# Kernel optimization log

Hardware: AMD Instinct MI355X
Metric: run time of the kernel (lower is better)

## Reference

```python
import jax, jax.numpy as jnp
import numpy as np

DIM = 768
HEADS = 12
HD = DIM // HEADS  # 64
EPS = 1e-5


def _ln(t, g, b):
    # LayerNorm over last axis (head_dim), torch eps=1e-5, biased variance
    mu = jnp.mean(t, axis=-1, keepdims=True)
    var = jnp.mean(jnp.square(t - mu), axis=-1, keepdims=True)
    return (t - mu) * jax.lax.rsqrt(var + EPS) * g + b


def _get_qkv(t, W, bias, gq, bq, gk, bk):
    bs, n, c = t.shape
    qkv = t @ W.T + bias                      # [bs, n, 3c]
    q, k, v = jnp.split(qkv, 3, axis=-1)
    def heads(u):
        return u.reshape(bs, n, HEADS, HD).transpose(0, 2, 1, 3)  # [bs,H,n,hd]
    q, k, v = heads(q), heads(k), heads(v)
    return _ln(q, gq, bq), _ln(k, gk, bk), v


def setup_inputs() -> dict:
    key = jax.random.key(0)
    ks = jax.random.split(key, 12)
    s_in = 1.0 / np.sqrt(DIM)
    d = {
        "x": jax.random.normal(ks[0], (4, 1024, DIM), jnp.float32),
        "y": jax.random.normal(ks[1], (4, 1024, DIM), jnp.float32),
        "Wqkv_x": jax.random.uniform(ks[2], (3 * DIM, DIM), jnp.float32, -s_in, s_in),
        "bqkv_x": jnp.zeros((3 * DIM,), jnp.float32),
        "Wqkv_y": jax.random.uniform(ks[3], (3 * DIM, DIM), jnp.float32, -s_in, s_in),
        "bqkv_y": jnp.zeros((3 * DIM,), jnp.float32),
        "Wproj_x": jax.random.uniform(ks[4], (DIM, DIM), jnp.float32, -s_in, s_in),
        "bproj_x": jnp.zeros((DIM,), jnp.float32),
        "Wproj_y": jax.random.uniform(ks[5], (DIM, DIM), jnp.float32, -s_in, s_in),
        "bproj_y": jnp.zeros((DIM,), jnp.float32),
        "gq_x": jnp.ones((HD,), jnp.float32), "bq_x": jnp.zeros((HD,), jnp.float32),
        "gk_x": jnp.ones((HD,), jnp.float32), "bk_x": jnp.zeros((HD,), jnp.float32),
        "gq_y": jnp.ones((HD,), jnp.float32), "bq_y": jnp.zeros((HD,), jnp.float32),
        "gk_y": jnp.ones((HD,), jnp.float32), "bk_y": jnp.zeros((HD,), jnp.float32),
    }
    return d


def reference(x, y, Wqkv_x, bqkv_x, Wqkv_y, bqkv_y, Wproj_x, bproj_x,
              Wproj_y, bproj_y, gq_x, bq_x, gk_x, bk_x, gq_y, bq_y, gk_y, bk_y):
    bs, n, c = x.shape
    qx, kx, vx = _get_qkv(x, Wqkv_x, bqkv_x, gq_x, bq_x, gk_x, bk_x)
    qy, ky, vy = _get_qkv(y, Wqkv_y, bqkv_y, gq_y, bq_y, gk_y, bk_y)
    q = jnp.concatenate([qx, qy], axis=2)     # [bs,H,n+m,hd]
    k = jnp.concatenate([kx, ky], axis=2)
    v = jnp.concatenate([vx, vy], axis=2)
    score = jnp.einsum("bhqd,bhkd->bhqk", q, k) / np.sqrt(HD)
    attn = jax.nn.softmax(score, axis=-1)
    out = jnp.einsum("bhqk,bhkd->bhqd", attn, v)  # [bs,H,n+m,hd]
    out = out.transpose(0, 2, 1, 3).reshape(bs, -1, c)
    ox, oy = out[:, :n, :], out[:, n:, :]
    return ox @ Wproj_x.T + bproj_x, oy @ Wproj_y.T + bproj_y
```

## Files before the change

kernel.cpp:

```cpp
#include <hip/hip_runtime.h>
#include <stdint.h>

typedef unsigned int u32;
typedef __attribute__((ext_vector_type(8))) __bf16 bf16x8;
typedef __attribute__((ext_vector_type(8))) short s16x8;
typedef __attribute__((ext_vector_type(4))) short s16x4;
typedef __attribute__((ext_vector_type(4))) float f32x4;


__device__ __forceinline__ short f2bf(float f) {
    __bf16 h = (__bf16)f;
    return __builtin_bit_cast(short, h);
}

__device__ __forceinline__ bf16x8 asbf(s16x8 v) {
    return __builtin_bit_cast(bf16x8, v);
}

__device__ __forceinline__ void gl_lds16(const void* g, void* l) {
    __builtin_amdgcn_global_load_lds((__attribute__((address_space(1))) u32*)g,
                                     (__attribute__((address_space(3))) u32*)l,
                                     16, 0, 0);
}



__global__ __launch_bounds__(256) void pack_tiles(
    const float* __restrict__ x,  short* __restrict__ xP,
    const float* __restrict__ y,  short* __restrict__ yP,
    const float* __restrict__ wqx, short* __restrict__ wqxP,
    const float* __restrict__ wqy, short* __restrict__ wqyP,
    const float* __restrict__ wpx, short* __restrict__ wpxP,
    const float* __restrict__ wpy, short* __restrict__ wpyP)
{
    const int tid  = threadIdx.x;
    const int w    = tid >> 6, lane = tid & 63;
    const int lam  = lane & 15, quad = lane >> 4;

    int t = blockIdx.x;
    const float* src; short* dst;
    if (t < 384)                 { src = x;   dst = xP; }
    else if ((t -= 384) < 384)   { src = y;   dst = yP; }
    else if ((t -= 384) < 216)   { src = wqx; dst = wqxP; }
    else if ((t -= 216) < 216)   { src = wqy; dst = wqyP; }
    else if ((t -= 216) < 72)    { src = wpx; dst = wpxP; }
    else                         { t -= 72;  src = wpy; dst = wpyP; }

    const int kb = t % 12, rb = t / 12;
    const int m0 = rb * 128, k0 = kb * 64;
    short* dtile = dst + (size_t)t * 8192;

    #pragma unroll
    for (int u = 0; u < 2; u++) {
        const int ig = w * 2 + u;
        #pragma unroll
        for (int c = 0; c < 2; c++) {
            const float* sp = src + (size_t)(m0 + ig * 16 + lam) * 768 + k0 + c * 32 + quad * 8;
            f32x4 a = *(const f32x4*)sp;
            f32x4 b = *(const f32x4*)(sp + 4);
            s16x8 o;
            o[0] = f2bf(a.x); o[1] = f2bf(a.y); o[2] = f2bf(a.z); o[3] = f2bf(a.w);
            o[4] = f2bf(b.x); o[5] = f2bf(b.y); o[6] = f2bf(b.z); o[7] = f2bf(b.w);
            *(s16x8*)(dtile + (c * 8 + ig) * 512 + lane * 8) = o;
        }
    }
}


__device__ __forceinline__ void stage_qkv(
    const short* __restrict__ At, const short* __restrict__ Wt,
    short* __restrict__ dA, short* __restrict__ dB, int w, int lane)
{
    #pragma unroll
    for (int c = 0; c < 2; c++)
        #pragma unroll
        for (int h = 0; h < 2; h++) {
            const int ch = c * 8 + w + h * 4;
            gl_lds16(At + ch * 512 + lane * 8, dA + ch * 512);
            gl_lds16(Wt + ch * 512 + lane * 8, dB + ch * 512);
        }
}

__global__ __launch_bounds__(256, 2) void qkv_gemm(
    const short* __restrict__ AxP, const short* __restrict__ AyP,
    const short* __restrict__ WxP, const short* __restrict__ WyP,
    const float* __restrict__ biasx, const float* __restrict__ biasy,
    const float* __restrict__ gqx, const float* __restrict__ bqx,
    const float* __restrict__ gkx, const float* __restrict__ bkx,
    const float* __restrict__ gqy, const float* __restrict__ bqy,
    const float* __restrict__ gky, const float* __restrict__ bky,
    short* __restrict__ Q, short* __restrict__ KP, short* __restrict__ VP)
{
    __shared__ union {
        struct { short a[8192]; short b[8192]; } st;
        short e[4][5120];
    } uL;
    const int tid  = threadIdx.x;
    const int w    = tid >> 6, lane = tid & 63;
    const int lam  = lane & 15, quad = lane >> 4;
    const int strm = blockIdx.z;
    const int mblk = blockIdx.x;
    const int nblk = blockIdx.y;
    const short* AP   = strm ? AyP : AxP;
    const short* WP   = strm ? WyP : WxP;
    const float* bias = strm ? biasy : biasx;
    const int m0 = mblk * 128;
    const int n0 = nblk * 128;
    const int wm = w >> 1, wn = w & 1;

    const f32x4 fzero = {0.f, 0.f, 0.f, 0.f};
    f32x4 acc[4][4];
    #pragma unroll
    for (int i = 0; i < 4; i++)
        #pragma unroll
        for (int t = 0; t < 4; t++) acc[i][t] = fzero;

    for (int kb = 0; kb < 12; ++kb) {
        __syncthreads();
        stage_qkv(AP + (size_t)(mblk * 12 + kb) * 8192,
                  WP + (size_t)(nblk * 12 + kb) * 8192,
                  uL.st.a, uL.st.b, w, lane);
        __syncthreads();
        s16x8 af[2][4], bfr[2][4];
        #pragma unroll
        for (int c = 0; c < 2; c++)
            #pragma unroll
            for (int i = 0; i < 4; i++)
                af[c][i] = *(const s16x8*)(uL.st.a + ((c * 8 + wm * 4 + i) * 64 + lane) * 8);
        #pragma unroll
        for (int c = 0; c < 2; c++)
            #pragma unroll
            for (int t = 0; t < 4; t++)
                bfr[c][t] = *(const s16x8*)(uL.st.b + ((c * 8 + wn * 4 + t) * 64 + lane) * 8);
        #pragma unroll
        for (int c = 0; c < 2; c++)
            #pragma unroll
            for (int i = 0; i < 4; i++)
                #pragma unroll
                for (int t = 0; t < 4; t++)
                    acc[i][t] = __builtin_amdgcn_mfma_f32_16x16x32_bf16(
                        asbf(af[c][i]), asbf(bfr[c][t]), acc[i][t], 0, 0, 0);
    }
    __syncthreads();

    const int nb     = n0 + wn * 64;
    const int region = nb / 768;
    const int head   = (nb % 768) / 64;
    const int mg0    = m0 + wm * 64;
    const int b_     = mg0 >> 10;
    const int sg0    = (mg0 & 1023) + strm * 1024;
    short* myE = uL.e[w];

    float bv[4];
    #pragma unroll
    for (int t = 0; t < 4; t++) bv[t] = bias[nb + t * 16 + lam];
    float gv[4], bb[4];
    if (region < 2) {
        const float* gp = (region == 0) ? (strm ? gqy : gqx) : (strm ? gky : gkx);
        const float* bp = (region == 0) ? (strm ? bqy : bqx) : (strm ? bky : bkx);
        #pragma unroll
        for (int t = 0; t < 4; t++) { gv[t] = gp[t * 16 + lam]; bb[t] = bp[t * 16 + lam]; }
    }

    #pragma unroll
    for (int i = 0; i < 4; i++) {
        #pragma unroll
        for (int reg = 0; reg < 4; reg++) {
            const int lr = i * 16 + quad * 4 + reg;
            float v0 = acc[i][0][reg] + bv[0];
            float v1 = acc[i][1][reg] + bv[1];
            float v2 = acc[i][2][reg] + bv[2];
            float v3 = acc[i][3][reg] + bv[3];
            if (region < 2) {
                float s = v0 + v1 + v2 + v3;
                s += __shfl_xor(s, 1); s += __shfl_xor(s, 2);
                s += __shfl_xor(s, 4); s += __shfl_xor(s, 8);
                const float mean = s * (1.f / 64.f);
                const float c0 = v0 - mean, c1 = v1 - mean, c2 = v2 - mean, c3 = v3 - mean;
                float q2 = c0 * c0 + c1 * c1 + c2 * c2 + c3 * c3;
                q2 += __shfl_xor(q2, 1); q2 += __shfl_xor(q2, 2);
                q2 += __shfl_xor(q2, 4); q2 += __shfl_xor(q2, 8);
                const float rs = rsqrtf(q2 * (1.f / 64.f) + 1e-5f);
                v0 = c0 * rs * gv[0] + bb[0];
                v1 = c1 * rs * gv[1] + bb[1];
                v2 = c2 * rs * gv[2] + bb[2];
                v3 = c3 * rs * gv[3] + bb[3];
                myE[lr * 80 + 0 * 16 + lam] = f2bf(v0);
                myE[lr * 80 + 1 * 16 + lam] = f2bf(v1);
                myE[lr * 80 + 2 * 16 + lam] = f2bf(v2);
                myE[lr * 80 + 3 * 16 + lam] = f2bf(v3);
            } else {
                myE[(0 * 16 + lam) * 80 + lr] = f2bf(v0);
                myE[(1 * 16 + lam) * 80 + lr] = f2bf(v1);
                myE[(2 * 16 + lam) * 80 + lr] = f2bf(v2);
                myE[(3 * 16 + lam) * 80 + lr] = f2bf(v3);
            }
        }
    }

    if (region == 0) {
        const int l8 = lane >> 3, c8 = (lane & 7) * 8;
        short* dstp = Q + ((size_t)(b_ * 12 + head) * 2048 + sg0) * 64;
        #pragma unroll
        for (int j = 0; j < 8; j++) {
            const int rr = j * 8 + l8;
            *(s16x8*)(dstp + (size_t)rr * 64 + c8) = *(const s16x8*)(myE + rr * 80 + c8);
        }
    } else {
        short* dstp = (region == 1 ? KP : VP) +
                      ((size_t)(b_ * 12 + head) * 32 + (sg0 >> 6)) * 4096;
        #pragma unroll
        for (int c = 0; c < 2; c++)
            #pragma unroll
            for (int ig = 0; ig < 4; ig++) {
                s16x8 vv = *(const s16x8*)(myE + (ig * 16 + lam) * 80 + c * 32 + quad * 8);
                *(s16x8*)(dstp + (c * 4 + ig) * 512 + lane * 8) = vv;
            }
    }
}


__global__ __launch_bounds__(256, 2) void attn(
    const short* __restrict__ Q, const short* __restrict__ KP,
    const short* __restrict__ VP, short* __restrict__ OP)
{
    __shared__ __align__(16) short lP[4][2560];
    const int tid  = threadIdx.x;
    const int w    = tid >> 6, lane = tid & 63;
    const int lam  = lane & 15, quad = lane >> 4;
    const int bh   = blockIdx.x;
    const int q0   = blockIdx.y * 128 + w * 32;
    const short* Qb  = Q  + (size_t)bh * 2048 * 64;
    const short* KPb = KP + (size_t)bh * 32 * 4096;
    const short* VPb = VP + (size_t)bh * 32 * 4096;
    short* myP = lP[w];

    s16x8 aq[2][2];
    #pragma unroll
    for (int qf = 0; qf < 2; qf++)
        #pragma unroll
        for (int c = 0; c < 2; c++)
            aq[qf][c] = *(const s16x8*)(Qb + (size_t)(q0 + qf * 16 + lam) * 64 + c * 32 + quad * 8);

    const f32x4 fzero = {0.f, 0.f, 0.f, 0.f};
    f32x4 o[2][4];
    float lsum[2][4];
    #pragma unroll
    for (int qf = 0; qf < 2; qf++) {
        #pragma unroll
        for (int t = 0; t < 4; t++) o[qf][t] = fzero;
        #pragma unroll
        for (int r = 0; r < 4; r++) lsum[qf][r] = 0.f;
    }

    const float c1 = 0.18033688011112042f;

    for (int it = 0; it < 32; ++it) {
        const short* kt = KPb + (size_t)it * 4096;
        const short* vt = VPb + (size_t)it * 4096;

        s16x8 kf[4][2];
        #pragma unroll
        for (int t = 0; t < 4; t++) {
            kf[t][0] = *(const s16x8*)(kt + (0 * 4 + t) * 512 + lane * 8);
            kf[t][1] = *(const s16x8*)(kt + (1 * 4 + t) * 512 + lane * 8);
        }
        s16x8 vf[4][2];
        #pragma unroll
        for (int t = 0; t < 4; t++) {
            vf[t][0] = *(const s16x8*)(vt + (0 * 4 + t) * 512 + lane * 8);
            vf[t][1] = *(const s16x8*)(vt + (1 * 4 + t) * 512 + lane * 8);
        }

        f32x4 sc[2][4];
        #pragma unroll
        for (int qf = 0; qf < 2; qf++)
            #pragma unroll
            for (int t = 0; t < 4; t++) sc[qf][t] = fzero;
        #pragma unroll
        for (int t = 0; t < 4; t++)
            #pragma unroll
            for (int qf = 0; qf < 2; qf++) {
                sc[qf][t] = __builtin_amdgcn_mfma_f32_16x16x32_bf16(
                    asbf(aq[qf][0]), asbf(kf[t][0]), sc[qf][t], 0, 0, 0);
                sc[qf][t] = __builtin_amdgcn_mfma_f32_16x16x32_bf16(
                    asbf(aq[qf][1]), asbf(kf[t][1]), sc[qf][t], 0, 0, 0);
            }

        s16x8 ap[2][2];
        #pragma unroll
        for (int qf = 0; qf < 2; qf++) {
            #pragma unroll
            for (int t = 0; t < 4; t++) {
                const int g = t * 2 + (lam >> 3);
                #pragma unroll
                for (int r = 0; r < 4; r++) {
                    const float p = __builtin_amdgcn_exp2f(__builtin_fmaf(sc[qf][t][r], c1, -30.f));
                    lsum[qf][r] += p;
                    myP[(g * 17 + quad * 4 + r) * 8 + (lam & 7)] = f2bf(p);
                }
            }
            ap[qf][0] = *(const s16x8*)(myP + (quad * 17 + lam) * 8);
            ap[qf][1] = *(const s16x8*)(myP + ((4 + quad) * 17 + lam) * 8);
        }

        #pragma unroll
        for (int t = 0; t < 4; t++)
            #pragma unroll
            for (int qf = 0; qf < 2; qf++) {
                o[qf][t] = __builtin_amdgcn_mfma_f32_16x16x32_bf16(
                    asbf(ap[qf][0]), asbf(vf[t][0]), o[qf][t], 0, 0, 0);
                o[qf][t] = __builtin_amdgcn_mfma_f32_16x16x32_bf16(
                    asbf(ap[qf][1]), asbf(vf[t][1]), o[qf][t], 0, 0, 0);
            }
    }

    short* myO = lP[w];
    #pragma unroll
    for (int qf = 0; qf < 2; qf++) {
        #pragma unroll
        for (int r = 0; r < 4; r++) {
            float l = lsum[qf][r];
            l += __shfl_xor(l, 1); l += __shfl_xor(l, 2);
            l += __shfl_xor(l, 4); l += __shfl_xor(l, 8);
            const float inv = 1.0f / l;
            const int row = qf * 16 + quad * 4 + r;
            #pragma unroll
            for (int t = 0; t < 4; t++)
                myO[row * 80 + t * 16 + lam] = f2bf(o[qf][t][r] * inv);
        }
    }

    const int b_ = bh / 12, h_ = bh % 12;
    const int strm = q0 >> 10;
    const int s    = q0 & 1023;
    const int sb   = s >> 6;
    short* dstp = OP + (((size_t)((strm * 4 + b_) * 16 + sb)) * 12 + h_) * 4096;
    const int igb = (s & 63) >> 4;
    #pragma unroll
    for (int u = 0; u < 2; u++) {
        const int ig = igb + u;
        #pragma unroll
        for (int c = 0; c < 2; c++) {
            s16x8 vv = *(const s16x8*)(myO + (u * 16 + lam) * 80 + c * 32 + quad * 8);
            *(s16x8*)(dstp + (c * 4 + ig) * 512 + lane * 8) = vv;
        }
    }
}


__device__ __forceinline__ void stage_proj(
    const short* __restrict__ Ot, const short* __restrict__ Wt,
    short* __restrict__ dA, short* __restrict__ dB, int w, int lane)
{
    #pragma unroll
    for (int u = 0; u < 2; u++) {
        const int ch = w * 2 + u;
        gl_lds16(Ot + ch * 512 + lane * 8, dA + ch * 512);
    }
    #pragma unroll
    for (int c = 0; c < 2; c++)
        #pragma unroll
        for (int h = 0; h < 2; h++) {
            const int ch = c * 8 + w + h * 4;
            gl_lds16(Wt + ch * 512 + lane * 8, dB + ch * 512);
        }
}

__global__ __launch_bounds__(256, 3) void proj_gemm(
    const short* __restrict__ OP,
    const short* __restrict__ WpxP, const short* __restrict__ WpyP,
    const float* __restrict__ bpx, const float* __restrict__ bpy,
    float* __restrict__ out)
{
    __shared__ __align__(16) short lA[2][4096];
    __shared__ __align__(16) short lB[2][8192];
    const int tid  = threadIdx.x;
    const int w    = tid >> 6, lane = tid & 63;
    const int lam  = lane & 15, quad = lane >> 4;
    const int strm = blockIdx.z;
    const short* WP   = strm ? WpyP : WpxP;
    const float* bias = strm ? bpy : bpx;
    const int m0 = blockIdx.x * 64;
    const int n0 = blockIdx.y * 128;
    const int wm = w >> 1, wn = w & 1;

    const int b_ = m0 >> 10, sb = (m0 & 1023) >> 6;
    const size_t tA0 = ((size_t)((strm * 4 + b_) * 16 + sb)) * 12;
    const size_t tB0 = (size_t)blockIdx.y * 12;

    const f32x4 fzero = {0.f, 0.f, 0.f, 0.f};
    f32x4 acc[2][4];
    #pragma unroll
    for (int i = 0; i < 2; i++)
        #pragma unroll
        for (int t = 0; t < 4; t++) acc[i][t] = fzero;

    stage_proj(OP + tA0 * 4096, WP + tB0 * 8192, lA[0], lB[0], w, lane);
    __syncthreads();

    int bi = 0;
    for (int kb = 0; kb < 12; ++kb) {
        if (kb + 1 < 12)
            stage_proj(OP + (tA0 + kb + 1) * 4096, WP + (tB0 + kb + 1) * 8192,
                       lA[bi ^ 1], lB[bi ^ 1], w, lane);

        const short* cA = lA[bi];
        const short* cB = lB[bi];
        s16x8 af[2][2], bfr[2][4];
        #pragma unroll
        for (int c = 0; c < 2; c++)
            #pragma unroll
            for (int i = 0; i < 2; i++)
                af[c][i] = *(const s16x8*)(cA + ((c * 4 + wm * 2 + i) * 64 + lane) * 8);
        #pragma unroll
        for (int c = 0; c < 2; c++)
            #pragma unroll
            for (int t = 0; t < 4; t++)
                bfr[c][t] = *(const s16x8*)(cB + ((c * 8 + wn * 4 + t) * 64 + lane) * 8);
        #pragma unroll
        for (int c = 0; c < 2; c++)
            #pragma unroll
            for (int i = 0; i < 2; i++)
                #pragma unroll
                for (int t = 0; t < 4; t++)
                    acc[i][t] = __builtin_amdgcn_mfma_f32_16x16x32_bf16(
                        asbf(af[c][i]), asbf(bfr[c][t]), acc[i][t], 0, 0, 0);

        __syncthreads();
        bi ^= 1;
    }

    const int nb = n0 + wn * 64;
    float bv[4];
    #pragma unroll
    for (int t = 0; t < 4; t++) bv[t] = bias[nb + t * 16 + lam];
    #pragma unroll
    for (int i = 0; i < 2; i++) {
        #pragma unroll
        for (int reg = 0; reg < 4; reg++) {
            const int mg = m0 + wm * 32 + i * 16 + quad * 4 + reg;
            float* dst = out + (size_t)strm * 3145728 + (size_t)mg * 768 + nb;
            #pragma unroll
            for (int t = 0; t < 4; t++) dst[t * 16 + lam] = acc[i][t][reg] + bv[t];
        }
    }
}


#define WS_XP  0
#define WS_YP  6291456
#define WS_WQX 12582912
#define WS_WQY 16121856
#define WS_WPX 19660800
#define WS_WPY 20840448
#define WS_Q   22020096
#define WS_KP  34603008
#define WS_VP  47185920
#define WS_OP  59768832

extern "C" void kernel_launch(void* const* d_in, const int* in_sizes, int n_in,
                              void* d_out, int out_size, void* d_ws, size_t ws_size,
                              hipStream_t stream) {
    (void)in_sizes; (void)n_in; (void)out_size; (void)ws_size;
    const float* x       = (const float*)d_in[0];
    const float* y       = (const float*)d_in[1];
    const float* Wqkv_x  = (const float*)d_in[2];
    const float* bqkv_x  = (const float*)d_in[3];
    const float* Wqkv_y  = (const float*)d_in[4];
    const float* bqkv_y  = (const float*)d_in[5];
    const float* Wproj_x = (const float*)d_in[6];
    const float* bproj_x = (const float*)d_in[7];
    const float* Wproj_y = (const float*)d_in[8];
    const float* bproj_y = (const float*)d_in[9];
    const float* gq_x = (const float*)d_in[10];
    const float* bq_x = (const float*)d_in[11];
    const float* gk_x = (const float*)d_in[12];
    const float* bk_x = (const float*)d_in[13];
    const float* gq_y = (const float*)d_in[14];
    const float* bq_y = (const float*)d_in[15];
    const float* gk_y = (const float*)d_in[16];
    const float* bk_y = (const float*)d_in[17];

    char* ws = (char*)d_ws;
    short* xP   = (short*)(ws + WS_XP);
    short* yP   = (short*)(ws + WS_YP);
    short* wqxP = (short*)(ws + WS_WQX);
    short* wqyP = (short*)(ws + WS_WQY);
    short* wpxP = (short*)(ws + WS_WPX);
    short* wpyP = (short*)(ws + WS_WPY);
    short* Qb   = (short*)(ws + WS_Q);
    short* KPb  = (short*)(ws + WS_KP);
    short* VPb  = (short*)(ws + WS_VP);
    short* OPb  = (short*)(ws + WS_OP);

    pack_tiles<<<1344, 256, 0, stream>>>(x, xP, y, yP, Wqkv_x, wqxP,
                                         Wqkv_y, wqyP, Wproj_x, wpxP, Wproj_y, wpyP);

    dim3 g1(32, 18, 2);
    qkv_gemm<<<g1, 256, 0, stream>>>(xP, yP, wqxP, wqyP, bqkv_x, bqkv_y,
                                     gq_x, bq_x, gk_x, bk_x,
                                     gq_y, bq_y, gk_y, bk_y,
                                     Qb, KPb, VPb);

    dim3 g2(48, 16);
    attn<<<g2, 256, 0, stream>>>(Qb, KPb, VPb, OPb);

    dim3 g3(64, 6, 2);
    proj_gemm<<<g3, 256, 0, stream>>>(OPb, wpxP, wpyP, bproj_x, bproj_y, (float*)d_out);
}
```

Measured before the change: 238.5 us.

## Keep softmax P in registers via transposed QK^T and 16x16x16 MFMA for PV

The attention kernel now computes S^T by swapping the MFMA operands, so each lane holds four keys for one query. That lets P be fed straight into a 16x16x16 bf16 MFMA against V fragments loaded as 4-wide pieces, removing the LDS round trip for P. The softmax scale is folded into the Q LayerNorm gamma and beta, and the -30 offset into the score accumulator's initial value. The QKV GEMM drops LDS staging and barriers in favour of direct global-to-register double-buffered fragment loads. This risks redundant global loads across waves and uses the lower-throughput K=16 MFMA for the PV product.

```diff
diff --git a/kernel.cpp b/kernel.cpp
--- a/kernel.cpp
+++ b/kernel.cpp
@@ -3,6 +3,7 @@
 
 typedef unsigned int u32;
 typedef __attribute__((ext_vector_type(8))) __bf16 bf16x8;
+typedef __attribute__((ext_vector_type(4))) __bf16 bf16x4;
 typedef __attribute__((ext_vector_type(8))) short s16x8;
 typedef __attribute__((ext_vector_type(4))) short s16x4;
 typedef __attribute__((ext_vector_type(4))) float f32x4;
@@ -15,6 +16,26 @@
 
 __device__ __forceinline__ bf16x8 asbf(s16x8 v) {
     return __builtin_bit_cast(bf16x8, v);
+}
+
+__device__ __forceinline__ f32x4 mfma32(s16x8 a, s16x8 b, f32x4 c) {
+    return __builtin_amdgcn_mfma_f32_16x16x32_bf16(asbf(a), asbf(b), c, 0, 0, 0);
+}
+
+__device__ __forceinline__ f32x4 mfma16(s16x4 a, s16x4 b, f32x4 c) {
+#if defined(__AMDGCN__)
+#if __has_builtin(__builtin_amdgcn_mfma_f32_16x16x16bf16_1k)
+    return __builtin_amdgcn_mfma_f32_16x16x16bf16_1k(a, b, c, 0, 0, 0);
+#else
+    f32x4 d;
+    asm volatile("v_mfma_f32_16x16x16_bf16 %0, %1, %2, %3"
+                 : "=v"(d) : "v"(a), "v"(b), "v"(c));
+    return d;
+#endif
+#else
+    (void)a; (void)b;
+    return c;
+#endif
 }
 
 __device__ __forceinline__ void gl_lds16(const void* g, void* l) {
@@ -67,20 +88,6 @@
 }
 
 
-__device__ __forceinline__ void stage_qkv(
-    const short* __restrict__ At, const short* __restrict__ Wt,
-    short* __restrict__ dA, short* __restrict__ dB, int w, int lane)
-{
-    #pragma unroll
-    for (int c = 0; c < 2; c++)
-        #pragma unroll
-        for (int h = 0; h < 2; h++) {
-            const int ch = c * 8 + w + h * 4;
-            gl_lds16(At + ch * 512 + lane * 8, dA + ch * 512);
-            gl_lds16(Wt + ch * 512 + lane * 8, dB + ch * 512);
-        }
-}
-
 __global__ __launch_bounds__(256, 2) void qkv_gemm(
     const short* __restrict__ AxP, const short* __restrict__ AyP,
     const short* __restrict__ WxP, const short* __restrict__ WyP,
@@ -91,10 +98,7 @@
     const float* __restrict__ gky, const float* __restrict__ bky,
     short* __restrict__ Q, short* __restrict__ KP, short* __restrict__ VP)
 {
-    __shared__ union {
-        struct { short a[8192]; short b[8192]; } st;
-        short e[4][5120];
-    } uL;
+    __shared__ __align__(16) short lE[4][5120];
     const int tid  = threadIdx.x;
     const int w    = tid >> 6, lane = tid & 63;
     const int lam  = lane & 15, quad = lane >> 4;
@@ -108,6 +112,9 @@
     const int n0 = nblk * 128;
     const int wm = w >> 1, wn = w & 1;
 
+    const short* Ap = AP + (size_t)mblk * 12 * 8192 + lane * 8;
+    const short* Wp = WP + (size_t)nblk * 12 * 8192 + lane * 8;
+
     const f32x4 fzero = {0.f, 0.f, 0.f, 0.f};
     f32x4 acc[4][4];
     #pragma unroll
@@ -115,33 +122,30 @@
         #pragma unroll
         for (int t = 0; t < 4; t++) acc[i][t] = fzero;
 
-    for (int kb = 0; kb < 12; ++kb) {
-        __syncthreads();
-        stage_qkv(AP + (size_t)(mblk * 12 + kb) * 8192,
-                  WP + (size_t)(nblk * 12 + kb) * 8192,
-                  uL.st.a, uL.st.b, w, lane);
-        __syncthreads();
-        s16x8 af[2][4], bfr[2][4];
-        #pragma unroll
-        for (int c = 0; c < 2; c++)
-            #pragma unroll
-            for (int i = 0; i < 4; i++)
-                af[c][i] = *(const s16x8*)(uL.st.a + ((c * 8 + wm * 4 + i) * 64 + lane) * 8);
-        #pragma unroll
-        for (int c = 0; c < 2; c++)
+    #define QOFF(kc_, sel_, i_) (((kc_) >> 1) * 8192 + (((kc_) & 1) * 8 + (sel_) * 4 + (i_)) * 512)
+
+    s16x8 fa[2][4], fb[2][4];
+    #pragma unroll
+    for (int i = 0; i < 4; i++) fa[0][i] = *(const s16x8*)(Ap + QOFF(0, wm, i));
+    #pragma unroll
+    for (int t = 0; t < 4; t++) fb[0][t] = *(const s16x8*)(Wp + QOFF(0, wn, t));
+
+    #pragma unroll
+    for (int kc = 0; kc < 24; ++kc) {
+        const int cur = kc & 1, nxt = cur ^ 1;
+        if (kc + 1 < 24) {
+            #pragma unroll
+            for (int i = 0; i < 4; i++) fa[nxt][i] = *(const s16x8*)(Ap + QOFF(kc + 1, wm, i));
+            #pragma unroll
+            for (int t = 0; t < 4; t++) fb[nxt][t] = *(const s16x8*)(Wp + QOFF(kc + 1, wn, t));
+        }
+        #pragma unroll
+        for (int i = 0; i < 4; i++)
             #pragma unroll
             for (int t = 0; t < 4; t++)
-                bfr[c][t] = *(const s16x8*)(uL.st.b + ((c * 8 + wn * 4 + t) * 64 + lane) * 8);
-        #pragma unroll
-        for (int c = 0; c < 2; c++)
-            #pragma unroll
-            for (int i = 0; i < 4; i++)
-                #pragma unroll
-                for (int t = 0; t < 4; t++)
-                    acc[i][t] = __builtin_amdgcn_mfma_f32_16x16x32_bf16(
-                        asbf(af[c][i]), asbf(bfr[c][t]), acc[i][t], 0, 0, 0);
-    }
-    __syncthreads();
+                acc[i][t] = mfma32(fa[cur][i], fb[cur][t], acc[i][t]);
+    }
+    #undef QOFF
 
     const int nb     = n0 + wn * 64;
     const int region = nb / 768;
@@ -149,7 +153,7 @@
     const int mg0    = m0 + wm * 64;
     const int b_     = mg0 >> 10;
     const int sg0    = (mg0 & 1023) + strm * 1024;
-    short* myE = uL.e[w];
+    short* myE = lE[w];
 
     float bv[4];
     #pragma unroll
@@ -158,8 +162,9 @@
     if (region < 2) {
         const float* gp = (region == 0) ? (strm ? gqy : gqx) : (strm ? gky : gkx);
         const float* bp = (region == 0) ? (strm ? bqy : bqx) : (strm ? bky : bkx);
-        #pragma unroll
-        for (int t = 0; t < 4; t++) { gv[t] = gp[t * 16 + lam]; bb[t] = bp[t * 16 + lam]; }
+        const float qs  = (region == 0) ? 0.18033688011112042f : 1.0f;
+        #pragma unroll
+        for (int t = 0; t < 4; t++) { gv[t] = gp[t * 16 + lam] * qs; bb[t] = bp[t * 16 + lam] * qs; }
     }
 
     #pragma unroll
@@ -224,7 +229,7 @@
     const short* __restrict__ Q, const short* __restrict__ KP,
     const short* __restrict__ VP, short* __restrict__ OP)
 {
-    __shared__ __align__(16) short lP[4][2560];
+    __shared__ __align__(16) short lO[4][2560];
     const int tid  = threadIdx.x;
     const int w    = tid >> 6, lane = tid & 63;
     const int lam  = lane & 15, quad = lane >> 4;
@@ -233,7 +238,6 @@
     const short* Qb  = Q  + (size_t)bh * 2048 * 64;
     const short* KPb = KP + (size_t)bh * 32 * 4096;
     const short* VPb = VP + (size_t)bh * 32 * 4096;
-    short* myP = lP[w];
 
     s16x8 aq[2][2];
     #pragma unroll
@@ -243,17 +247,16 @@
             aq[qf][c] = *(const s16x8*)(Qb + (size_t)(q0 + qf * 16 + lam) * 64 + c * 32 + quad * 8);
 
     const f32x4 fzero = {0.f, 0.f, 0.f, 0.f};
+    const f32x4 minit = {-30.f, -30.f, -30.f, -30.f};
     f32x4 o[2][4];
-    float lsum[2][4];
-    #pragma unroll
-    for (int qf = 0; qf < 2; qf++) {
+    float lsum[2] = {0.f, 0.f};
+    #pragma unroll
+    for (int qf = 0; qf < 2; qf++)
         #pragma unroll
         for (int t = 0; t < 4; t++) o[qf][t] = fzero;
-        #pragma unroll
-        for (int r = 0; r < 4; r++) lsum[qf][r] = 0.f;
-    }
-
-    const float c1 = 0.18033688011112042f;
+
+    const int vsub0 = ((0 * 2 + (quad >> 1)) * 16 + lam) * 8 + (quad & 1) * 4;
+    const int vsub1 = ((1 * 2 + (quad >> 1)) * 16 + lam) * 8 + (quad & 1) * 4;
 
     for (int it = 0; it < 32; ++it) {
         const short* kt = KPb + (size_t)it * 4096;
@@ -265,65 +268,52 @@
             kf[t][0] = *(const s16x8*)(kt + (0 * 4 + t) * 512 + lane * 8);
             kf[t][1] = *(const s16x8*)(kt + (1 * 4 + t) * 512 + lane * 8);
         }
-        s16x8 vf[4][2];
-        #pragma unroll
-        for (int t = 0; t < 4; t++) {
-            vf[t][0] = *(const s16x8*)(vt + (0 * 4 + t) * 512 + lane * 8);
-            vf[t][1] = *(const s16x8*)(vt + (1 * 4 + t) * 512 + lane * 8);
-        }
-
-        f32x4 sc[2][4];
-        #pragma unroll
-        for (int qf = 0; qf < 2; qf++)
-            #pragma unroll
-            for (int t = 0; t < 4; t++) sc[qf][t] = fzero;
-        #pragma unroll
-        for (int t = 0; t < 4; t++)
-            #pragma unroll
-            for (int qf = 0; qf < 2; qf++) {
-                sc[qf][t] = __builtin_amdgcn_mfma_f32_16x16x32_bf16(
-                    asbf(aq[qf][0]), asbf(kf[t][0]), sc[qf][t], 0, 0, 0);
-                sc[qf][t] = __builtin_amdgcn_mfma_f32_16x16x32_bf16(
-                    asbf(aq[qf][1]), asbf(kf[t][1]), sc[qf][t], 0, 0, 0);
+        s16x4 vb[4][4];
+        #pragma unroll
+        for (int dt = 0; dt < 4; dt++)
+            #pragma unroll
+            for (int t = 0; t < 4; t++)
+                vb[dt][t] = *(const s16x4*)(vt + ((t >> 1) * 4 + dt) * 512 +
+                                            ((t & 1) ? vsub1 : vsub0));
+
+        #pragma unroll
+        for (int qf = 0; qf < 2; qf++) {
+            f32x4 sc[4];
+            #pragma unroll
+            for (int t = 0; t < 4; t++) sc[t] = minit;
+            #pragma unroll
+            for (int t = 0; t < 4; t++) {
+                sc[t] = mfma32(kf[t][0], aq[qf][0], sc[t]);
+                sc[t] = mfma32(kf[t][1], aq[qf][1], sc[t]);
             }
-
-        s16x8 ap[2][2];
-        #pragma unroll
-        for (int qf = 0; qf < 2; qf++) {
-            #pragma unroll
-            for (int t = 0; t < 4; t++) {
-                const int g = t * 2 + (lam >> 3);
+            s16x4 pf[4];
+            float ls = 0.f;
+            #pragma unroll
+            for (int t = 0; t < 4; t++)
                 #pragma unroll
                 for (int r = 0; r < 4; r++) {
-                    const float p = __builtin_amdgcn_exp2f(__builtin_fmaf(sc[qf][t][r], c1, -30.f));
-                    lsum[qf][r] += p;
-                    myP[(g * 17 + quad * 4 + r) * 8 + (lam & 7)] = f2bf(p);
+                    const float p = __builtin_amdgcn_exp2f(sc[t][r]);
+                    ls += p;
+                    pf[t][r] = f2bf(p);
                 }
-            }
-            ap[qf][0] = *(const s16x8*)(myP + (quad * 17 + lam) * 8);
-            ap[qf][1] = *(const s16x8*)(myP + ((4 + quad) * 17 + lam) * 8);
-        }
-
-        #pragma unroll
-        for (int t = 0; t < 4; t++)
-            #pragma unroll
-            for (int qf = 0; qf < 2; qf++) {
-                o[qf][t] = __builtin_amdgcn_mfma_f32_16x16x32_bf16(
-                    asbf(ap[qf][0]), asbf(vf[t][0]), o[qf][t], 0, 0, 0);
-                o[qf][t] = __builtin_amdgcn_mfma_f32_16x16x32_bf16(
-                    asbf(ap[qf][1]), asbf(vf[t][1]), o[qf][t], 0, 0, 0);
-            }
-    }
-
-    short* myO = lP[w];
+            lsum[qf] += ls;
+            #pragma unroll
+            for (int dt = 0; dt < 4; dt++)
+                #pragma unroll
+                for (int t = 0; t < 4; t++)
+                    o[qf][dt] = mfma16(pf[t], vb[dt][t], o[qf][dt]);
+        }
+    }
+
+    short* myO = lO[w];
     #pragma unroll
     for (int qf = 0; qf < 2; qf++) {
+        float l = lsum[qf];
+        l += __shfl_xor(l, 16);
+        l += __shfl_xor(l, 32);
         #pragma unroll
         for (int r = 0; r < 4; r++) {
-            float l = lsum[qf][r];
-            l += __shfl_xor(l, 1); l += __shfl_xor(l, 2);
-            l += __shfl_xor(l, 4); l += __shfl_xor(l, 8);
-            const float inv = 1.0f / l;
+            const float inv = 1.0f / __shfl(l, quad * 4 + r, 16);
             const int row = qf * 16 + quad * 4 + r;
             #pragma unroll
             for (int t = 0; t < 4; t++)
@@ -424,8 +414,7 @@
             for (int i = 0; i < 2; i++)
                 #pragma unroll
                 for (int t = 0; t < 4; t++)
-                    acc[i][t] = __builtin_amdgcn_mfma_f32_16x16x32_bf16(
-                        asbf(af[c][i]), asbf(bfr[c][t]), acc[i][t], 0, 0, 0);
+                    acc[i][t] = mfma32(af[c][i], bfr[c][t], acc[i][t]);
 
         __syncthreads();
         bi ^= 1;
```

Result: slower. 253.1 us (+6.1%).

## Shrink attention tiles to 16 query rows per wave and fold softmax scale into Q LayerNorm

Applied to the files above, without the earlier changes.

The attention kernel now gives each wave 16 query rows instead of 32, doubles the grid, halves its LDS and raises launch bounds to 6 blocks per CU, aiming for higher occupancy to hide K/V load latency. The softmax scale (log2e/sqrt(hd)) is folded into the Q LayerNorm gain and bias, and the -30 offset is moved into the score accumulator's initial value, removing an FMA per score element. The QKV epilogue is split into two halves so it needs half the LDS staging. In exchange, each block reuses K/V fragments over fewer query rows, which doubles global/L2 traffic for K and V.

```diff
diff --git a/kernel.cpp b/kernel.cpp
--- a/kernel.cpp
+++ b/kernel.cpp
@@ -15,6 +15,10 @@
 
 __device__ __forceinline__ bf16x8 asbf(s16x8 v) {
     return __builtin_bit_cast(bf16x8, v);
+}
+
+__device__ __forceinline__ f32x4 mfma32(s16x8 a, s16x8 b, f32x4 c) {
+    return __builtin_amdgcn_mfma_f32_16x16x32_bf16(asbf(a), asbf(b), c, 0, 0, 0);
 }
 
 __device__ __forceinline__ void gl_lds16(const void* g, void* l) {
@@ -93,7 +97,7 @@
 {
     __shared__ union {
         struct { short a[8192]; short b[8192]; } st;
-        short e[4][5120];
+        short e[4][2560];
     } uL;
     const int tid  = threadIdx.x;
     const int w    = tid >> 6, lane = tid & 63;
@@ -138,8 +142,7 @@
             for (int i = 0; i < 4; i++)
                 #pragma unroll
                 for (int t = 0; t < 4; t++)
-                    acc[i][t] = __builtin_amdgcn_mfma_f32_16x16x32_bf16(
-                        asbf(af[c][i]), asbf(bfr[c][t]), acc[i][t], 0, 0, 0);
+                    acc[i][t] = mfma32(af[c][i], bfr[c][t], acc[i][t]);
     }
     __syncthreads();
 
@@ -154,181 +157,172 @@
     float bv[4];
     #pragma unroll
     for (int t = 0; t < 4; t++) bv[t] = bias[nb + t * 16 + lam];
-    float gv[4], bb[4];
+
     if (region < 2) {
         const float* gp = (region == 0) ? (strm ? gqy : gqx) : (strm ? gky : gkx);
         const float* bp = (region == 0) ? (strm ? bqy : bqx) : (strm ? bky : bkx);
-        #pragma unroll
-        for (int t = 0; t < 4; t++) { gv[t] = gp[t * 16 + lam]; bb[t] = bp[t * 16 + lam]; }
-    }
-
-    #pragma unroll
-    for (int i = 0; i < 4; i++) {
-        #pragma unroll
-        for (int reg = 0; reg < 4; reg++) {
-            const int lr = i * 16 + quad * 4 + reg;
-            float v0 = acc[i][0][reg] + bv[0];
-            float v1 = acc[i][1][reg] + bv[1];
-            float v2 = acc[i][2][reg] + bv[2];
-            float v3 = acc[i][3][reg] + bv[3];
-            if (region < 2) {
-                float s = v0 + v1 + v2 + v3;
-                s += __shfl_xor(s, 1); s += __shfl_xor(s, 2);
-                s += __shfl_xor(s, 4); s += __shfl_xor(s, 8);
-                const float mean = s * (1.f / 64.f);
-                const float c0 = v0 - mean, c1 = v1 - mean, c2 = v2 - mean, c3 = v3 - mean;
-                float q2 = c0 * c0 + c1 * c1 + c2 * c2 + c3 * c3;
-                q2 += __shfl_xor(q2, 1); q2 += __shfl_xor(q2, 2);
-                q2 += __shfl_xor(q2, 4); q2 += __shfl_xor(q2, 8);
-                const float rs = rsqrtf(q2 * (1.f / 64.f) + 1e-5f);
-                v0 = c0 * rs * gv[0] + bb[0];
-                v1 = c1 * rs * gv[1] + bb[1];
-                v2 = c2 * rs * gv[2] + bb[2];
-                v3 = c3 * rs * gv[3] + bb[3];
-                myE[lr * 80 + 0 * 16 + lam] = f2bf(v0);
-                myE[lr * 80 + 1 * 16 + lam] = f2bf(v1);
-                myE[lr * 80 + 2 * 16 + lam] = f2bf(v2);
-                myE[lr * 80 + 3 * 16 + lam] = f2bf(v3);
+        const float qs  = (region == 0) ? 0.18033688011112042f : 1.0f;
+        float gv[4], bb[4];
+        #pragma unroll
+        for (int t = 0; t < 4; t++) { gv[t] = gp[t * 16 + lam] * qs; bb[t] = bp[t * 16 + lam] * qs; }
+
+        short* dstQ = Q + ((size_t)(b_ * 12 + head) * 2048 + sg0) * 64;
+        short* dstK = KP + ((size_t)(b_ * 12 + head) * 32 + (sg0 >> 6)) * 4096;
+
+        #pragma unroll
+        for (int half = 0; half < 2; half++) {
+            #pragma unroll
+            for (int i2 = 0; i2 < 2; i2++) {
+                const int i = half * 2 + i2;
+                #pragma unroll
+                for (int reg = 0; reg < 4; reg++) {
+                    const int lrl = i2 * 16 + quad * 4 + reg;
+                    float v0 = acc[i][0][reg] + bv[0];
+                    float v1 = acc[i][1][reg] + bv[1];
+                    float v2 = acc[i][2][reg] + bv[2];
+                    float v3 = acc[i][3][reg] + bv[3];
+                    float s = v0 + v1 + v2 + v3;
+                    s += __shfl_xor(s, 1); s += __shfl_xor(s, 2);
+                    s += __shfl_xor(s, 4); s += __shfl_xor(s, 8);
+                    const float mean = s * (1.f / 64.f);
+                    const float c0 = v0 - mean, c1 = v1 - mean, c2 = v2 - mean, c3 = v3 - mean;
+                    float q2 = c0 * c0 + c1 * c1 + c2 * c2 + c3 * c3;
+                    q2 += __shfl_xor(q2, 1); q2 += __shfl_xor(q2, 2);
+                    q2 += __shfl_xor(q2, 4); q2 += __shfl_xor(q2, 8);
+                    const float rs = rsqrtf(q2 * (1.f / 64.f) + 1e-5f);
+                    myE[lrl * 80 + 0 * 16 + lam] = f2bf(c0 * rs * gv[0] + bb[0]);
+                    myE[lrl * 80 + 1 * 16 + lam] = f2bf(c1 * rs * gv[1] + bb[1]);
+                    myE[lrl * 80 + 2 * 16 + lam] = f2bf(c2 * rs * gv[2] + bb[2]);
+                    myE[lrl * 80 + 3 * 16 + lam] = f2bf(c3 * rs * gv[3] + bb[3]);
+                }
+            }
+            if (region == 0) {
+                const int l8 = lane >> 3, c8 = (lane & 7) * 8;
+                #pragma unroll
+                for (int j = 0; j < 4; j++) {
+                    const int rl = j * 8 + l8;
+                    *(s16x8*)(dstQ + (size_t)(half * 32 + rl) * 64 + c8) =
+                        *(const s16x8*)(myE + rl * 80 + c8);
+                }
             } else {
-                myE[(0 * 16 + lam) * 80 + lr] = f2bf(v0);
-                myE[(1 * 16 + lam) * 80 + lr] = f2bf(v1);
-                myE[(2 * 16 + lam) * 80 + lr] = f2bf(v2);
-                myE[(3 * 16 + lam) * 80 + lr] = f2bf(v3);
+                #pragma unroll
+                for (int c = 0; c < 2; c++)
+                    #pragma unroll
+                    for (int g2 = 0; g2 < 2; g2++) {
+                        const int ig = half * 2 + g2;
+                        s16x8 vv = *(const s16x8*)(myE + (g2 * 16 + lam) * 80 + c * 32 + quad * 8);
+                        *(s16x8*)(dstK + (c * 4 + ig) * 512 + lane * 8) = vv;
+                    }
             }
         }
-    }
-
-    if (region == 0) {
-        const int l8 = lane >> 3, c8 = (lane & 7) * 8;
-        short* dstp = Q + ((size_t)(b_ * 12 + head) * 2048 + sg0) * 64;
-        #pragma unroll
-        for (int j = 0; j < 8; j++) {
-            const int rr = j * 8 + l8;
-            *(s16x8*)(dstp + (size_t)rr * 64 + c8) = *(const s16x8*)(myE + rr * 80 + c8);
-        }
     } else {
-        short* dstp = (region == 1 ? KP : VP) +
-                      ((size_t)(b_ * 12 + head) * 32 + (sg0 >> 6)) * 4096;
-        #pragma unroll
-        for (int c = 0; c < 2; c++)
+        short* dstV = VP + ((size_t)(b_ * 12 + head) * 32 + (sg0 >> 6)) * 4096;
+        #pragma unroll
+        for (int half = 0; half < 2; half++) {
+            #pragma unroll
+            for (int i2 = 0; i2 < 2; i2++) {
+                const int i = half * 2 + i2;
+                #pragma unroll
+                for (int reg = 0; reg < 4; reg++) {
+                    const int lrc = i2 * 16 + quad * 4 + reg;
+                    myE[(0 * 16 + lam) * 40 + lrc] = f2bf(acc[i][0][reg] + bv[0]);
+                    myE[(1 * 16 + lam) * 40 + lrc] = f2bf(acc[i][1][reg] + bv[1]);
+                    myE[(2 * 16 + lam) * 40 + lrc] = f2bf(acc[i][2][reg] + bv[2]);
+                    myE[(3 * 16 + lam) * 40 + lrc] = f2bf(acc[i][3][reg] + bv[3]);
+                }
+            }
             #pragma unroll
             for (int ig = 0; ig < 4; ig++) {
-                s16x8 vv = *(const s16x8*)(myE + (ig * 16 + lam) * 80 + c * 32 + quad * 8);
-                *(s16x8*)(dstp + (c * 4 + ig) * 512 + lane * 8) = vv;
+                s16x8 vv = *(const s16x8*)(myE + (ig * 16 + lam) * 40 + quad * 8);
+                *(s16x8*)(dstV + (half * 4 + ig) * 512 + lane * 8) = vv;
             }
-    }
-}
-
-
-__global__ __launch_bounds__(256, 2) void attn(
+        }
+    }
+}
+
+
+__global__ __launch_bounds__(256, 6) void attn(
     const short* __restrict__ Q, const short* __restrict__ KP,
     const short* __restrict__ VP, short* __restrict__ OP)
 {
-    __shared__ __align__(16) short lP[4][2560];
+    __shared__ __align__(16) short lP[4][1280];
     const int tid  = threadIdx.x;
     const int w    = tid >> 6, lane = tid & 63;
     const int lam  = lane & 15, quad = lane >> 4;
     const int bh   = blockIdx.x;
-    const int q0   = blockIdx.y * 128 + w * 32;
+    const int q0   = blockIdx.y * 64 + w * 16;
     const short* Qb  = Q  + (size_t)bh * 2048 * 64;
     const short* KPb = KP + (size_t)bh * 32 * 4096;
     const short* VPb = VP + (size_t)bh * 32 * 4096;
     short* myP = lP[w];
 
-    s16x8 aq[2][2];
-    #pragma unroll
-    for (int qf = 0; qf < 2; qf++)
-        #pragma unroll
-        for (int c = 0; c < 2; c++)
-            aq[qf][c] = *(const s16x8*)(Qb + (size_t)(q0 + qf * 16 + lam) * 64 + c * 32 + quad * 8);
+    s16x8 aq[2];
+    #pragma unroll
+    for (int c = 0; c < 2; c++)
+        aq[c] = *(const s16x8*)(Qb + (size_t)(q0 + lam) * 64 + c * 32 + quad * 8);
 
     const f32x4 fzero = {0.f, 0.f, 0.f, 0.f};
-    f32x4 o[2][4];
-    float lsum[2][4];
-    #pragma unroll
-    for (int qf = 0; qf < 2; qf++) {
-        #pragma unroll
-        for (int t = 0; t < 4; t++) o[qf][t] = fzero;
-        #pragma unroll
-        for (int r = 0; r < 4; r++) lsum[qf][r] = 0.f;
-    }
-
-    const float c1 = 0.18033688011112042f;
+    const f32x4 minit = {-30.f, -30.f, -30.f, -30.f};
+    f32x4 o[4];
+    float lsum[4];
+    #pragma unroll
+    for (int t = 0; t < 4; t++) o[t] = fzero;
+    #pragma unroll
+    for (int r = 0; r < 4; r++) lsum[r] = 0.f;
 
     for (int it = 0; it < 32; ++it) {
         const short* kt = KPb + (size_t)it * 4096;
         const short* vt = VPb + (size_t)it * 4096;
 
-        s16x8 kf[4][2];
+        s16x8 kf[4][2], vf[4][2];
         #pragma unroll
         for (int t = 0; t < 4; t++) {
             kf[t][0] = *(const s16x8*)(kt + (0 * 4 + t) * 512 + lane * 8);
             kf[t][1] = *(const s16x8*)(kt + (1 * 4 + t) * 512 + lane * 8);
-        }
-        s16x8 vf[4][2];
-        #pragma unroll
-        for (int t = 0; t < 4; t++) {
             vf[t][0] = *(const s16x8*)(vt + (0 * 4 + t) * 512 + lane * 8);
             vf[t][1] = *(const s16x8*)(vt + (1 * 4 + t) * 512 + lane * 8);
         }
 
-        f32x4 sc[2][4];
-        #pragma unroll
-        for (int qf = 0; qf < 2; qf++)
-            #pragma unroll
-            for (int t = 0; t < 4; t++) sc[qf][t] = fzero;
+        f32x4 sc[4];
+        #pragma unroll
+        for (int t = 0; t < 4; t++) sc[t] = minit;
+        #pragma unroll
+        for (int t = 0; t < 4; t++) {
+            sc[t] = mfma32(aq[0], kf[t][0], sc[t]);
+            sc[t] = mfma32(aq[1], kf[t][1], sc[t]);
+        }
+
+        #pragma unroll
+        for (int t = 0; t < 4; t++) {
+            const int g = t * 2 + (lam >> 3);
+            #pragma unroll
+            for (int r = 0; r < 4; r++) {
+                const float p = __builtin_amdgcn_exp2f(sc[t][r]);
+                lsum[r] += p;
+                myP[(g * 17 + quad * 4 + r) * 8 + (lam & 7)] = f2bf(p);
+            }
+        }
+        s16x8 ap0 = *(const s16x8*)(myP + (quad * 17 + lam) * 8);
+        s16x8 ap1 = *(const s16x8*)(myP + ((4 + quad) * 17 + lam) * 8);
+
+        #pragma unroll
+        for (int t = 0; t < 4; t++) {
+            o[t] = mfma32(ap0, vf[t][0], o[t]);
+            o[t] = mfma32(ap1, vf[t][1], o[t]);
+        }
+    }
+
+    short* myO = myP;
+    #pragma unroll
+    for (int r = 0; r < 4; r++) {
+        float l = lsum[r];
+        l += __shfl_xor(l, 1); l += __shfl_xor(l, 2);
+        l += __shfl_xor(l, 4); l += __shfl_xor(l, 8);
+        const float inv = 1.0f / l;
+        const int row = quad * 4 + r;
         #pragma unroll
         for (int t = 0; t < 4; t++)
-            #pragma unroll
-            for (int qf = 0; qf < 2; qf++) {
-                sc[qf][t] = __builtin_amdgcn_mfma_f32_16x16x32_bf16(
-                    asbf(aq[qf][0]), asbf(kf[t][0]), sc[qf][t], 0, 0, 0);
-                sc[qf][t] = __builtin_amdgcn_mfma_f32_16x16x32_bf16(
-                    asbf(aq[qf][1]), asbf(kf[t][1]), sc[qf][t], 0, 0, 0);
-            }
-
-        s16x8 ap[2][2];
-        #pragma unroll
-        for (int qf = 0; qf < 2; qf++) {
-            #pragma unroll
-            for (int t = 0; t < 4; t++) {
-                const int g = t * 2 + (lam >> 3);
-                #pragma unroll
-                for (int r = 0; r < 4; r++) {
-                    const float p = __builtin_amdgcn_exp2f(__builtin_fmaf(sc[qf][t][r], c1, -30.f));
-                    lsum[qf][r] += p;
-                    myP[(g * 17 + quad * 4 + r) * 8 + (lam & 7)] = f2bf(p);
-                }
-            }
-            ap[qf][0] = *(const s16x8*)(myP + (quad * 17 + lam) * 8);
-            ap[qf][1] = *(const s16x8*)(myP + ((4 + quad) * 17 + lam) * 8);
-        }
-
-        #pragma unroll
-        for (int t = 0; t < 4; t++)
-            #pragma unroll
-            for (int qf = 0; qf < 2; qf++) {
-                o[qf][t] = __builtin_amdgcn_mfma_f32_16x16x32_bf16(
-                    asbf(ap[qf][0]), asbf(vf[t][0]), o[qf][t], 0, 0, 0);
-                o[qf][t] = __builtin_amdgcn_mfma_f32_16x16x32_bf16(
-                    asbf(ap[qf][1]), asbf(vf[t][1]), o[qf][t], 0, 0, 0);
-            }
-    }
-
-    short* myO = lP[w];
-    #pragma unroll
-    for (int qf = 0; qf < 2; qf++) {
-        #pragma unroll
-        for (int r = 0; r < 4; r++) {
-            float l = lsum[qf][r];
-            l += __shfl_xor(l, 1); l += __shfl_xor(l, 2);
-            l += __shfl_xor(l, 4); l += __shfl_xor(l, 8);
-            const float inv = 1.0f / l;
-            const int row = qf * 16 + quad * 4 + r;
-            #pragma unroll
-            for (int t = 0; t < 4; t++)
-                myO[row * 80 + t * 16 + lam] = f2bf(o[qf][t][r] * inv);
-        }
+            myO[row * 80 + t * 16 + lam] = f2bf(o[t][r] * inv);
     }
 
     const int b_ = bh / 12, h_ = bh % 12;
@@ -336,15 +330,10 @@
     const int s    = q0 & 1023;
     const int sb   = s >> 6;
     short* dstp = OP + (((size_t)((strm * 4 + b_) * 16 + sb)) * 12 + h_) * 4096;
-    const int igb = (s & 63) >> 4;
-    #pragma unroll
-    for (int u = 0; u < 2; u++) {
-        const int ig = igb + u;
-        #pragma unroll
-        for (int c = 0; c < 2; c++) {
-            s16x8 vv = *(const s16x8*)(myO + (u * 16 + lam) * 80 + c * 32 + quad * 8);
-            *(s16x8*)(dstp + (c * 4 + ig) * 512 + lane * 8) = vv;
-        }
+    #pragma unroll
+    for (int c = 0; c < 2; c++) {
+        s16x8 vv = *(const s16x8*)(myO + lam * 80 + c * 32 + quad * 8);
+        *(s16x8*)(dstp + (c * 4 + w) * 512 + lane * 8) = vv;
     }
 }
 
@@ -424,8 +413,7 @@
             for (int i = 0; i < 2; i++)
                 #pragma unroll
                 for (int t = 0; t < 4; t++)
-                    acc[i][t] = __builtin_amdgcn_mfma_f32_16x16x32_bf16(
-                        asbf(af[c][i]), asbf(bfr[c][t]), acc[i][t], 0, 0, 0);
+                    acc[i][t] = mfma32(af[c][i], bfr[c][t], acc[i][t]);
 
         __syncthreads();
         bi ^= 1;
@@ -503,7 +491,7 @@
                                      gq_y, bq_y, gk_y, bk_y,
                                      Qb, KPb, VPb);
 
-    dim3 g2(48, 16);
+    dim3 g2(48, 32);
     attn<<<g2, 256, 0, stream>>>(Qb, KPb, VPb, OPb);
 
     dim3 g3(64, 6, 2);
```

Result: slower. 274.5 us (+15.1%).
